# Kernel optimization log

Measured on AMD Instinct MI355X. Metric: run time of the kernel, lower is better.

## Reference

```python
import jax, jax.numpy as jnp
import numpy as np
from jax import lax

B, C, F, T = 32, 1, 128, 8000
FLOOR = 1e-06


def setup_inputs() -> dict:
    key = jax.random.key(0)
    mag_spec = jax.random.uniform(key, (B, C, F, T), dtype=jnp.float32)  # non-negative magnitudes
    alpha = jnp.full((C,), 0.96, dtype=jnp.float32)
    delta = jnp.full((C,), 2.0, dtype=jnp.float32)
    root = jnp.full((C,), 2.0, dtype=jnp.float32)
    smooth = jnp.full((1,), 0.04, dtype=jnp.float32)  # per_channel_smoothing=False -> shape (1,)
    return {"mag_spec": mag_spec, "alpha": alpha, "delta": delta, "root": root, "smooth": smooth}


def reference(mag_spec, alpha, delta, root, smooth):
    # mag_spec: [B, C, F, T]
    w = jnp.clip(smooth, 0.0, 1.0)[:, None]          # broadcast over (C, F) per time-step
    xs = jnp.moveaxis(mag_spec, -1, 0)               # [T, B, C, F]
    init = xs[0]                                     # initial_state = mag_spec[..., 0]

    def step(acc, x):
        acc = w * x + (1.0 - w) * acc
        return acc, acc

    final, ema = lax.scan(step, init, xs)            # ema: [T, B, C, F]
    ema = jnp.moveaxis(ema, 0, -1)                   # [B, C, F, T]

    a = jnp.minimum(alpha, 1.0)[:, None, None]       # (C,1,1) -> broadcast over F,T
    d = delta[:, None, None]
    one_over_root = 1.0 / jnp.maximum(root, 1.0)[:, None, None]

    out = (mag_spec / (FLOOR + ema) ** a + d) ** one_over_root - d ** one_over_root
    hidden_state = final[..., None]                  # [B, C, F, 1]
    return out, hidden_state
```

## Files before the change

kernel.cpp:

```cpp
#include <hip/hip_runtime.h>

#define FLOOR_EPS 1e-6f

typedef float floatx4 __attribute__((ext_vector_type(4)));

constexpr int Bq = 32, Cq = 1, Fq = 128, Tq = 8000;
constexpr int ROWS  = Bq * Cq * Fq;
constexpr int LPR   = 8;
constexpr int RNDE  = 64 * LPR;
constexpr int SPLIT = 4;
constexpr int MAIN  = Tq / SPLIT;
constexpr int NRM   = (MAIN + RNDE - 1) / RNDE;
constexpr int LACT  = (MAIN - (NRM - 1) * RNDE) / LPR;
constexpr int WPB   = 4;
constexpr unsigned TOTE = (unsigned)ROWS * Tq;

__global__ __launch_bounds__(256)
void _PCEN_75033078661345_kernel(const float* __restrict__ x,
                                 const float* __restrict__ alpha,
                                 const float* __restrict__ delta,
                                 const float* __restrict__ root,
                                 const float* __restrict__ smooth,
                                 float* __restrict__ out,
                                 float* __restrict__ hid)
{
    const int lane = threadIdx.x & 63;
    const int wid  = threadIdx.x >> 6;
    const int gw   = blockIdx.x * WPB + wid;
    const int r    = gw >> 2;
    const int h    = gw & 3;
    const int c    = (r / Fq) % Cq;

    const float w   = fminf(fmaxf(smooth[0], 0.f), 1.f);
    const float om  = 1.f - w;
    const float aa  = fminf(alpha[c], 1.f);
    const float dd  = delta[c];
    const float oor = 1.f / fmaxf(root[c], 1.f);
    const bool  us  = (oor == 0.5f);
    const float droot = us ? __builtin_amdgcn_sqrtf(dd)
                           : __builtin_amdgcn_exp2f(oor * __builtin_amdgcn_logf(dd));

    float om2 = om * om, om4 = om2 * om2;
    float omp[6];
    omp[0] = om4 * om4;
    #pragma unroll
    for (int k = 1; k < 6; ++k) omp[k] = omp[k - 1] * omp[k - 1];
    float om8i = 1.f;
    #pragma unroll
    for (int k = 0; k < 6; ++k) om8i = ((lane >> k) & 1) ? om8i * omp[k] : om8i;
    const float omR = omp[5] * omp[5];

    int Rw = 0;
    if (h) {
        const float nl2 = fmaxf(-__builtin_amdgcn_logf(om), 1e-9f);
        float need = 30.f / (512.f * nl2);
        int ri = (int)ceilf(need);
        const int cap = (h * MAIN) / RNDE;
        Rw = ri < 1 ? 1 : ri;
        Rw = Rw > 3 ? 3 : Rw;
        Rw = Rw > cap ? cap : Rw;
    }
    const int w0 = h * MAIN - Rw * RNDE;
    const int nr = NRM + Rw;

    const unsigned rowbase = (unsigned)r * (unsigned)Tq;

    float carry = x[rowbase + (unsigned)w0];
    float accv  = 0.f;

    auto LOADR = [&](int sidx, float4& d0, float4& d1) {
        unsigned u = rowbase + (unsigned)(w0 + sidx * RNDE + lane * LPR);
        u = u > (TOTE - LPR) ? (TOTE - LPR) : u;
        const float4* p = (const float4*)(x + u);
        d0 = p[0]; d1 = p[1];
    };

    auto ROUND = [&](int sidx, float4 c0, float4 c1) {
        const float xv[LPR] = {c0.x, c0.y, c0.z, c0.w, c1.x, c1.y, c1.z, c1.w};
        float b = 0.f;
        #pragma unroll
        for (int j = 0; j < LPR; ++j) b = w * xv[j] + om * b;
        #pragma unroll
        for (int k = 0; k < 6; ++k) {
            const float pb = __shfl_up(b, 1 << k);
            const float nb = fmaf(omp[k], pb, b);
            b = (lane >= (1 << k)) ? nb : b;
        }
        const float pb1  = __shfl_up(b, 1);
        const float bex  = (lane == 0) ? 0.f : pb1;
        float acc        = fmaf(om8i, carry, bex);
        const float btot = __shfl(b, 63);
        carry = fmaf(omR, carry, btot);
        if (sidx >= Rw) {
            float ov[LPR];
            #pragma unroll
            for (int j = 0; j < LPR; ++j) {
                acc = w * xv[j] + om * acc;
                const float dp = __builtin_amdgcn_exp2f(-aa * __builtin_amdgcn_logf(FLOOR_EPS + acc));
                const float tt = fmaf(xv[j], dp, dd);
                ov[j] = us ? (__builtin_amdgcn_sqrtf(tt) - droot)
                           : (__builtin_amdgcn_exp2f(oor * __builtin_amdgcn_logf(tt)) - droot);
            }
            const bool lastr = (sidx == nr - 1);
            if (!lastr || lane < LACT) {
                floatx4* q = (floatx4*)(out + rowbase + (unsigned)(w0 + sidx * RNDE + lane * LPR));
                floatx4 o0 = {ov[0], ov[1], ov[2], ov[3]};
                floatx4 o1 = {ov[4], ov[5], ov[6], ov[7]};
                __builtin_nontemporal_store(o0, q);
                __builtin_nontemporal_store(o1, q + 1);
            }
            accv = acc;
        }
    };

    float4 A0, A1, B0, B1;
    LOADR(0, A0, A1);
    LOADR(1, B0, B1);
    int s = 0;
    for (; s + 1 < nr; s += 2) {
        float4 c0 = A0, c1 = A1;
        if (s + 2 < nr) LOADR(s + 2, A0, A1);
        ROUND(s, c0, c1);
        c0 = B0; c1 = B1;
        if (s + 3 < nr) LOADR(s + 3, B0, B1);
        ROUND(s + 1, c0, c1);
    }
    if (s < nr) ROUND(s, A0, A1);

    const float hh = __shfl(accv, LACT - 1);
    if (h == SPLIT - 1 && lane == 0) hid[r] = hh;
}

extern "C" void kernel_launch(void* const* d_in, const int* in_sizes, int n_in,
                              void* d_out, int out_size, void* d_ws, size_t ws_size,
                              hipStream_t stream) {
    const float* x      = (const float*)d_in[0];
    const float* alpha  = (const float*)d_in[1];
    const float* delta  = (const float*)d_in[2];
    const float* root   = (const float*)d_in[3];
    const float* smooth = (const float*)d_in[4];
    float* out = (float*)d_out;
    float* hid = out + (size_t)ROWS * Tq;

    _PCEN_75033078661345_kernel<<<(ROWS * SPLIT) / WPB, 256, 0, stream>>>(
        x, alpha, delta, root, smooth, out, hid);
}
```

Baseline: 53.95 us.

## Process two row segments per wave to interleave independent scan chains

```diff
diff --git a/kernel.cpp b/kernel.cpp
--- a/kernel.cpp
+++ b/kernel.cpp
@@ -13,6 +13,8 @@
 constexpr int NRM   = (MAIN + RNDE - 1) / RNDE;
 constexpr int LACT  = (MAIN - (NRM - 1) * RNDE) / LPR;
 constexpr int WPB   = 4;
+constexpr int NSEG  = ROWS * SPLIT;
+constexpr int NWAVE = NSEG / 2;
 constexpr unsigned TOTE = (unsigned)ROWS * Tq;
 
 __global__ __launch_bounds__(256)
@@ -27,15 +29,15 @@
     const int lane = threadIdx.x & 63;
     const int wid  = threadIdx.x >> 6;
     const int gw   = blockIdx.x * WPB + wid;
-    const int r    = gw >> 2;
-    const int h    = gw & 3;
-    const int c    = (r / Fq) % Cq;
+    const int h  = gw & 3;
+    const int rA = gw >> 2;
+    const int rB = rA + (NWAVE >> 2);
 
     const float w   = fminf(fmaxf(smooth[0], 0.f), 1.f);
     const float om  = 1.f - w;
-    const float aa  = fminf(alpha[c], 1.f);
-    const float dd  = delta[c];
-    const float oor = 1.f / fmaxf(root[c], 1.f);
+    const float aa  = fminf(alpha[0], 1.f);
+    const float dd  = delta[0];
+    const float oor = 1.f / fmaxf(root[0], 1.f);
     const bool  us  = (oor == 0.5f);
     const float droot = us ? __builtin_amdgcn_sqrtf(dd)
                            : __builtin_amdgcn_exp2f(oor * __builtin_amdgcn_logf(dd));
@@ -63,19 +65,22 @@
     const int w0 = h * MAIN - Rw * RNDE;
     const int nr = NRM + Rw;
 
-    const unsigned rowbase = (unsigned)r * (unsigned)Tq;
+    const unsigned baseA = (unsigned)rA * (unsigned)Tq;
+    const unsigned baseB = (unsigned)rB * (unsigned)Tq;
 
-    float carry = x[rowbase + (unsigned)w0];
-    float accv  = 0.f;
+    float carryA = x[baseA + (unsigned)w0];
+    float carryB = x[baseB + (unsigned)w0];
+    float accA = 0.f, accB = 0.f;
 
-    auto LOADR = [&](int sidx, float4& d0, float4& d1) {
-        unsigned u = rowbase + (unsigned)(w0 + sidx * RNDE + lane * LPR);
+    auto LOADR = [&](unsigned base, int sidx, float4& d0, float4& d1) {
+        unsigned u = base + (unsigned)(w0 + sidx * RNDE + lane * LPR);
         u = u > (TOTE - LPR) ? (TOTE - LPR) : u;
         const float4* p = (const float4*)(x + u);
         d0 = p[0]; d1 = p[1];
     };
 
-    auto ROUND = [&](int sidx, float4 c0, float4 c1) {
+    auto ROUND = [&](unsigned base, int sidx, float4 c0, float4 c1,
+                     float& carry, float& accv) {
         const float xv[LPR] = {c0.x, c0.y, c0.z, c0.w, c1.x, c1.y, c1.z, c1.w};
         float b = 0.f;
         #pragma unroll
@@ -103,7 +108,7 @@
             }
             const bool lastr = (sidx == nr - 1);
             if (!lastr || lane < LACT) {
-                floatx4* q = (floatx4*)(out + rowbase + (unsigned)(w0 + sidx * RNDE + lane * LPR));
+                floatx4* q = (floatx4*)(out + base + (unsigned)(w0 + sidx * RNDE + lane * LPR));
                 floatx4 o0 = {ov[0], ov[1], ov[2], ov[3]};
                 floatx4 o1 = {ov[4], ov[5], ov[6], ov[7]};
                 __builtin_nontemporal_store(o0, q);
@@ -113,22 +118,29 @@
         }
     };
 
-    float4 A0, A1, B0, B1;
-    LOADR(0, A0, A1);
-    LOADR(1, B0, B1);
+    float4 XA0, XA1, XB0, XB1;
+    float4 YA0, YA1, YB0, YB1;
+    LOADR(baseA, 0, XA0, XA1);  LOADR(baseB, 0, YA0, YA1);
+    LOADR(baseA, 1, XB0, XB1);  LOADR(baseB, 1, YB0, YB1);
     int s = 0;
     for (; s + 1 < nr; s += 2) {
-        float4 c0 = A0, c1 = A1;
-        if (s + 2 < nr) LOADR(s + 2, A0, A1);
-        ROUND(s, c0, c1);
-        c0 = B0; c1 = B1;
-        if (s + 3 < nr) LOADR(s + 3, B0, B1);
-        ROUND(s + 1, c0, c1);
+        float4 a0 = XA0, a1 = XA1, b0 = YA0, b1 = YA1;
+        if (s + 2 < nr) { LOADR(baseA, s + 2, XA0, XA1); LOADR(baseB, s + 2, YA0, YA1); }
+        ROUND(baseA, s, a0, a1, carryA, accA);
+        ROUND(baseB, s, b0, b1, carryB, accB);
+        a0 = XB0; a1 = XB1; b0 = YB0; b1 = YB1;
+        if (s + 3 < nr) { LOADR(baseA, s + 3, XB0, XB1); LOADR(baseB, s + 3, YB0, YB1); }
+        ROUND(baseA, s + 1, a0, a1, carryA, accA);
+        ROUND(baseB, s + 1, b0, b1, carryB, accB);
     }
-    if (s < nr) ROUND(s, A0, A1);
+    if (s < nr) {
+        ROUND(baseA, s, XA0, XA1, carryA, accA);
+        ROUND(baseB, s, YA0, YA1, carryB, accB);
+    }
 
-    const float hh = __shfl(accv, LACT - 1);
-    if (h == SPLIT - 1 && lane == 0) hid[r] = hh;
+    const float hA = __shfl(accA, LACT - 1);
+    const float hB = __shfl(accB, LACT - 1);
+    if (h == SPLIT - 1 && lane == 0) { hid[rA] = hA; hid[rB] = hB; }
 }
 
 extern "C" void kernel_launch(void* const* d_in, const int* in_sizes, int n_in,
@@ -142,6 +154,6 @@
     float* out = (float*)d_out;
     float* hid = out + (size_t)ROWS * Tq;
 
-    _PCEN_75033078661345_kernel<<<(ROWS * SPLIT) / WPB, 256, 0, stream>>>(
+    _PCEN_75033078661345_kernel<<<NWAVE / WPB, 256, 0, stream>>>(
         x, alpha, delta, root, smooth, out, hid);
 }
```

Result: slower. 55.66 us (+3.2%).

## Widen per-lane chunk to 16 elements and unroll round loop explicitly

Applied to the files above, without the earlier changes.

```diff
diff --git a/kernel.cpp b/kernel.cpp
--- a/kernel.cpp
+++ b/kernel.cpp
@@ -2,17 +2,16 @@
 
 #define FLOOR_EPS 1e-6f
 
-typedef float floatx4 __attribute__((ext_vector_type(4)));
-
 constexpr int Bq = 32, Cq = 1, Fq = 128, Tq = 8000;
 constexpr int ROWS  = Bq * Cq * Fq;
-constexpr int LPR   = 8;
+constexpr int LPR   = 16;
 constexpr int RNDE  = 64 * LPR;
 constexpr int SPLIT = 4;
 constexpr int MAIN  = Tq / SPLIT;
 constexpr int NRM   = (MAIN + RNDE - 1) / RNDE;
 constexpr int LACT  = (MAIN - (NRM - 1) * RNDE) / LPR;
 constexpr int WPB   = 4;
+constexpr int NSEG  = ROWS * SPLIT;
 constexpr unsigned TOTE = (unsigned)ROWS * Tq;
 
 __global__ __launch_bounds__(256)
@@ -25,39 +24,35 @@
                                  float* __restrict__ hid)
 {
     const int lane = threadIdx.x & 63;
-    const int wid  = threadIdx.x >> 6;
-    const int gw   = blockIdx.x * WPB + wid;
-    const int r    = gw >> 2;
-    const int h    = gw & 3;
-    const int c    = (r / Fq) % Cq;
+    const int h    = threadIdx.x >> 6;
+    const int r    = blockIdx.x;
 
     const float w   = fminf(fmaxf(smooth[0], 0.f), 1.f);
     const float om  = 1.f - w;
-    const float aa  = fminf(alpha[c], 1.f);
-    const float dd  = delta[c];
-    const float oor = 1.f / fmaxf(root[c], 1.f);
+    const float aa  = fminf(alpha[0], 1.f);
+    const float dd  = delta[0];
+    const float oor = 1.f / fmaxf(root[0], 1.f);
     const bool  us  = (oor == 0.5f);
     const float droot = us ? __builtin_amdgcn_sqrtf(dd)
                            : __builtin_amdgcn_exp2f(oor * __builtin_amdgcn_logf(dd));
 
-    float om2 = om * om, om4 = om2 * om2;
+    float om2 = om * om, om4 = om2 * om2, om8 = om4 * om4;
     float omp[6];
-    omp[0] = om4 * om4;
+    omp[0] = om8 * om8;
     #pragma unroll
     for (int k = 1; k < 6; ++k) omp[k] = omp[k - 1] * omp[k - 1];
-    float om8i = 1.f;
+    float om16i = 1.f;
     #pragma unroll
-    for (int k = 0; k < 6; ++k) om8i = ((lane >> k) & 1) ? om8i * omp[k] : om8i;
+    for (int k = 0; k < 6; ++k) om16i = ((lane >> k) & 1) ? om16i * omp[k] : om16i;
     const float omR = omp[5] * omp[5];
 
     int Rw = 0;
     if (h) {
         const float nl2 = fmaxf(-__builtin_amdgcn_logf(om), 1e-9f);
-        float need = 30.f / (512.f * nl2);
-        int ri = (int)ceilf(need);
+        int ri = (int)ceilf(30.f / (1024.f * nl2));
         const int cap = (h * MAIN) / RNDE;
         Rw = ri < 1 ? 1 : ri;
-        Rw = Rw > 3 ? 3 : Rw;
+        Rw = Rw > 2 ? 2 : Rw;
         Rw = Rw > cap ? cap : Rw;
     }
     const int w0 = h * MAIN - Rw * RNDE;
@@ -68,15 +63,16 @@
     float carry = x[rowbase + (unsigned)w0];
     float accv  = 0.f;
 
-    auto LOADR = [&](int sidx, float4& d0, float4& d1) {
+    auto LOADR = [&](int sidx, float4& d0, float4& d1, float4& d2, float4& d3) {
         unsigned u = rowbase + (unsigned)(w0 + sidx * RNDE + lane * LPR);
         u = u > (TOTE - LPR) ? (TOTE - LPR) : u;
         const float4* p = (const float4*)(x + u);
-        d0 = p[0]; d1 = p[1];
+        d0 = p[0]; d1 = p[1]; d2 = p[2]; d3 = p[3];
     };
 
-    auto ROUND = [&](int sidx, float4 c0, float4 c1) {
-        const float xv[LPR] = {c0.x, c0.y, c0.z, c0.w, c1.x, c1.y, c1.z, c1.w};
+    auto ROUND = [&](int sidx, float4 c0, float4 c1, float4 c2, float4 c3) {
+        const float xv[LPR] = {c0.x, c0.y, c0.z, c0.w, c1.x, c1.y, c1.z, c1.w,
+                               c2.x, c2.y, c2.z, c2.w, c3.x, c3.y, c3.z, c3.w};
         float b = 0.f;
         #pragma unroll
         for (int j = 0; j < LPR; ++j) b = w * xv[j] + om * b;
@@ -88,7 +84,7 @@
         }
         const float pb1  = __shfl_up(b, 1);
         const float bex  = (lane == 0) ? 0.f : pb1;
-        float acc        = fmaf(om8i, carry, bex);
+        float acc        = fmaf(om16i, carry, bex);
         const float btot = __shfl(b, 63);
         carry = fmaf(omR, carry, btot);
         if (sidx >= Rw) {
@@ -103,29 +99,33 @@
             }
             const bool lastr = (sidx == nr - 1);
             if (!lastr || lane < LACT) {
-                floatx4* q = (floatx4*)(out + rowbase + (unsigned)(w0 + sidx * RNDE + lane * LPR));
-                floatx4 o0 = {ov[0], ov[1], ov[2], ov[3]};
-                floatx4 o1 = {ov[4], ov[5], ov[6], ov[7]};
-                __builtin_nontemporal_store(o0, q);
-                __builtin_nontemporal_store(o1, q + 1);
+                float4* q = (float4*)(out + rowbase + (unsigned)(w0 + sidx * RNDE + lane * LPR));
+                q[0] = {ov[0],  ov[1],  ov[2],  ov[3]};
+                q[1] = {ov[4],  ov[5],  ov[6],  ov[7]};
+                q[2] = {ov[8],  ov[9],  ov[10], ov[11]};
+                q[3] = {ov[12], ov[13], ov[14], ov[15]};
             }
             accv = acc;
         }
     };
 
-    float4 A0, A1, B0, B1;
-    LOADR(0, A0, A1);
-    LOADR(1, B0, B1);
-    int s = 0;
-    for (; s + 1 < nr; s += 2) {
-        float4 c0 = A0, c1 = A1;
-        if (s + 2 < nr) LOADR(s + 2, A0, A1);
-        ROUND(s, c0, c1);
-        c0 = B0; c1 = B1;
-        if (s + 3 < nr) LOADR(s + 3, B0, B1);
-        ROUND(s + 1, c0, c1);
+    float4 A0, A1, A2, A3, B0, B1, B2, B3;
+    LOADR(0, A0, A1, A2, A3);
+    LOADR(1, B0, B1, B2, B3);
+    ROUND(0, A0, A1, A2, A3);
+    if (nr == 2) {
+        ROUND(1, B0, B1, B2, B3);
+    } else if (nr == 3) {
+        LOADR(2, A0, A1, A2, A3);
+        ROUND(1, B0, B1, B2, B3);
+        ROUND(2, A0, A1, A2, A3);
+    } else {
+        LOADR(2, A0, A1, A2, A3);
+        ROUND(1, B0, B1, B2, B3);
+        LOADR(3, B0, B1, B2, B3);
+        ROUND(2, A0, A1, A2, A3);
+        ROUND(3, B0, B1, B2, B3);
     }
-    if (s < nr) ROUND(s, A0, A1);
 
     const float hh = __shfl(accv, LACT - 1);
     if (h == SPLIT - 1 && lane == 0) hid[r] = hh;
@@ -142,6 +142,6 @@
     float* out = (float*)d_out;
     float* hid = out + (size_t)ROWS * Tq;
 
-    _PCEN_75033078661345_kernel<<<(ROWS * SPLIT) / WPB, 256, 0, stream>>>(
+    _PCEN_75033078661345_kernel<<<NSEG / WPB, 256, 0, stream>>>(
         x, alpha, delta, root, smooth, out, hid);
 }
```

Result: slower. 61.24 us (+13.5%).
